# Kernel tuning notes

Hardware: AMD Instinct MI355X
Metric: run time of the kernel (lower is better)

Reference implementation:

```python
import jax, jax.numpy as jnp
import numpy as np


def setup_inputs() -> dict:
    key = jax.random.key(0)
    k1, k2, k3 = jax.random.split(key, 3)
    B, N, D = 32, 1024, 256  # batch, seq len (shared), window_len
    t = jax.random.normal(k1, (B, N, D), dtype=jnp.float32)
    f = jax.random.normal(k2, (B, N, D), dtype=jnp.float32)
    W = jax.random.normal(k3, (D, D), dtype=jnp.float32)  # nn.init.normal_(std=1)
    return {"t": t, "f": f, "W": W}


def reference(t, f, W):
    # s_weight[b,n,m] = t[b,n,:] @ W @ f[b,m,:]
    tW = jnp.einsum('bnd,de->bne', t, W)          # [B,N,D]
    s_weight = jnp.einsum('bne,bme->bnm', tW, f)  # [B,N,N]
    t_weight = jax.nn.softmax(s_weight, axis=1)   # softmax over L_t (dim=1)
    f_weight = jax.nn.softmax(s_weight, axis=2)   # softmax over L_f (dim=2)
    # t_out = t^T @ t_weight -> [B,D,N]
    t_out = jnp.einsum('bnd,bnm->bdm', t, t_weight)
    # f_out = f^T @ f_weight -> [B,D,N] (requires L_t == L_f)
    f_out = jnp.einsum('bmd,bmk->bdk', f, f_weight)
    # Dropout(0.3) omitted (eval-mode identity) for deterministic reference.
    return (t_out, f_out)
```

## Files before the change

kernel.cpp:

```cpp
#include <hip/hip_runtime.h>
#include <math.h>

#define BB 32
#define NN 1024
#define DD 256
#define CH 8
#define KSTEP 32
#define LDK 40

typedef __attribute__((ext_vector_type(8))) short short8;
typedef __attribute__((ext_vector_type(8))) unsigned short u16x8;
typedef __attribute__((ext_vector_type(4))) float f32x4;

__device__ __forceinline__ unsigned short f2bf(float x) {
  unsigned u = __float_as_uint(x);
  unsigned r = (u + 0x7fffu + ((u >> 16) & 1u)) >> 16;
  return (unsigned short)r;
}
__device__ __forceinline__ float bf2f(unsigned short h) {
  return __uint_as_float((unsigned)h << 16);
}

__global__ __launch_bounds__(256) void k_split(const float* __restrict__ src,
                                               unsigned short* __restrict__ hi,
                                               unsigned short* __restrict__ lo, int n4) {
  int i = blockIdx.x * 256 + threadIdx.x;
  if (i >= n4) return;
  float4 v = ((const float4*)src)[i];
  float xs[4] = {v.x, v.y, v.z, v.w};
  ushort4 h4, l4;
  unsigned short* hp = (unsigned short*)&h4;
  unsigned short* lp = (unsigned short*)&l4;
  #pragma unroll
  for (int j = 0; j < 4; ++j) {
    unsigned short h = f2bf(xs[j]);
    hp[j] = h;
    lp[j] = f2bf(xs[j] - bf2f(h));
  }
  ((ushort4*)hi)[i] = h4;
  ((ushort4*)lo)[i] = l4;
}

__global__ __launch_bounds__(256) void k_splitW(const float* __restrict__ W,
                                                unsigned short* __restrict__ Wth,
                                                unsigned short* __restrict__ Wtl) {
  int k = blockIdx.x, n = threadIdx.x;
  float x = W[k * DD + n];
  unsigned short h = f2bf(x);
  Wth[n * DD + k] = h;
  Wtl[n * DD + k] = f2bf(x - bf2f(h));
}

template <int EPI>
__global__ __launch_bounds__(256) void k_gemm_nt(const unsigned short* __restrict__ Ahg,
                                                 const unsigned short* __restrict__ Alg,
                                                 const unsigned short* __restrict__ Bhg,
                                                 const unsigned short* __restrict__ Blg,
                                                 unsigned short* __restrict__ outh,
                                                 unsigned short* __restrict__ outl,
                                                 float* __restrict__ outf, int b0) {
  size_t aoff = 0, boff = 0, coff = 0;
  int ldC = 256;
  if (EPI == 1) {
    int b = b0 + blockIdx.z;
    aoff = (size_t)b * NN * DD;
    boff = (size_t)b * NN * DD;
    coff = (size_t)blockIdx.z * NN * NN;
    ldC = NN;
  }
  const int n0 = blockIdx.x * 128, m0 = blockIdx.y * 128;
  __shared__ unsigned short Ah[128][LDK], Al[128][LDK], Bh[128][LDK], Bl[128][LDK];
  const int tid = threadIdx.x;
  const int lane = tid & 63, w = tid >> 6;
  const int wr = (w >> 1) * 64, wc = (w & 1) * 64;
  const int sr = tid >> 1, sk = (tid & 1) * 16;

  f32x4 acc[4][4] = {};
  const int fr = lane & 15, fk = (lane >> 4) * 8;

  for (int k0 = 0; k0 < DD; k0 += KSTEP) {
    const size_t abase = aoff + (size_t)(n0 + sr) * DD + k0 + sk;
    const size_t bbase = boff + (size_t)(m0 + sr) * DD + k0 + sk;
    *(u16x8*)&Ah[sr][sk] = *(const u16x8*)&Ahg[abase];
    *(u16x8*)&Ah[sr][sk + 8] = *(const u16x8*)&Ahg[abase + 8];
    *(u16x8*)&Al[sr][sk] = *(const u16x8*)&Alg[abase];
    *(u16x8*)&Al[sr][sk + 8] = *(const u16x8*)&Alg[abase + 8];
    *(u16x8*)&Bh[sr][sk] = *(const u16x8*)&Bhg[bbase];
    *(u16x8*)&Bh[sr][sk + 8] = *(const u16x8*)&Bhg[bbase + 8];
    *(u16x8*)&Bl[sr][sk] = *(const u16x8*)&Blg[bbase];
    *(u16x8*)&Bl[sr][sk + 8] = *(const u16x8*)&Blg[bbase + 8];
    __syncthreads();
    short8 ah[4], al[4], bh[4], bl[4];
    #pragma unroll
    for (int mi = 0; mi < 4; ++mi) {
      ah[mi] = *(const short8*)&Ah[wr + mi * 16 + fr][fk];
      al[mi] = *(const short8*)&Al[wr + mi * 16 + fr][fk];
    }
    #pragma unroll
    for (int ni = 0; ni < 4; ++ni) {
      bh[ni] = *(const short8*)&Bh[wc + ni * 16 + fr][fk];
      bl[ni] = *(const short8*)&Bl[wc + ni * 16 + fr][fk];
    }
    #pragma unroll
    for (int mi = 0; mi < 4; ++mi)
      #pragma unroll
      for (int ni = 0; ni < 4; ++ni) {
        acc[mi][ni] = __builtin_amdgcn_mfma_f32_16x16x32_bf16(ah[mi], bh[ni], acc[mi][ni], 0, 0, 0);
        acc[mi][ni] = __builtin_amdgcn_mfma_f32_16x16x32_bf16(ah[mi], bl[ni], acc[mi][ni], 0, 0, 0);
        acc[mi][ni] = __builtin_amdgcn_mfma_f32_16x16x32_bf16(al[mi], bh[ni], acc[mi][ni], 0, 0, 0);
      }
    __syncthreads();
  }
  const int fq = (lane >> 4) * 4;
  #pragma unroll
  for (int mi = 0; mi < 4; ++mi)
    #pragma unroll
    for (int ni = 0; ni < 4; ++ni) {
      #pragma unroll
      for (int q = 0; q < 4; ++q) {
        int row = n0 + wr + mi * 16 + fq + q;
        int col = m0 + wc + ni * 16 + fr;
        float x = acc[mi][ni][q];
        if (EPI == 0) {
          unsigned short h = f2bf(x);
          outh[(size_t)row * 256 + col] = h;
          outl[(size_t)row * 256 + col] = f2bf(x - bf2f(h));
        } else {
          outf[coff + (size_t)row * ldC + col] = x;
        }
      }
    }
}

__global__ __launch_bounds__(256) void k_rowstats(const float* __restrict__ s,
                                                  float* __restrict__ lr, int b0) {
  const int g = blockIdx.y, b = b0 + g, n = blockIdx.x;
  const float* row = s + (size_t)g * NN * NN + (size_t)n * NN;
  const int tid = threadIdx.x;
  float4 v = ((const float4*)row)[tid];
  float mx = fmaxf(fmaxf(v.x, v.y), fmaxf(v.z, v.w));
  float sum = __expf(v.x - mx) + __expf(v.y - mx) + __expf(v.z - mx) + __expf(v.w - mx);
  __shared__ float sm[256], ss[256];
  sm[tid] = mx; ss[tid] = sum;
  __syncthreads();
  for (int off = 128; off > 0; off >>= 1) {
    if (tid < off) {
      float m2 = sm[tid + off], s2 = ss[tid + off];
      float nm = fmaxf(sm[tid], m2);
      ss[tid] = ss[tid] * __expf(sm[tid] - nm) + s2 * __expf(m2 - nm);
      sm[tid] = nm;
    }
    __syncthreads();
  }
  if (tid == 0) lr[(size_t)b * NN + n] = sm[0] + __logf(ss[0]);
}

__global__ __launch_bounds__(256) void k_colstats_part(const float* __restrict__ s,
                                                       float* __restrict__ pm,
                                                       float* __restrict__ ps) {
  const int g = blockIdx.z, ch = blockIdx.y;
  const int mcol = blockIdx.x * 256 + threadIdx.x;
  const float* S = s + (size_t)g * NN * NN;
  float mx = -INFINITY, sum = 0.f;
  const int n0 = ch * (NN / CH), n1 = n0 + NN / CH;
  for (int n = n0; n < n1; ++n) {
    float x = S[(size_t)n * NN + mcol];
    float nm = fmaxf(mx, x);
    sum = sum * __expf(mx - nm) + __expf(x - nm);
    mx = nm;
  }
  pm[((size_t)g * CH + ch) * NN + mcol] = mx;
  ps[((size_t)g * CH + ch) * NN + mcol] = sum;
}

__global__ __launch_bounds__(256) void k_colstats_comb(const float* __restrict__ pm,
                                                       const float* __restrict__ ps,
                                                       float* __restrict__ lc, int b0) {
  const int g = blockIdx.y, b = b0 + g;
  const int mcol = blockIdx.x * 256 + threadIdx.x;
  float mx = -INFINITY, sum = 0.f;
  for (int ch = 0; ch < CH; ++ch) {
    float m2 = pm[((size_t)g * CH + ch) * NN + mcol];
    float s2 = ps[((size_t)g * CH + ch) * NN + mcol];
    float nm = fmaxf(mx, m2);
    sum = sum * __expf(mx - nm) + s2 * __expf(m2 - nm);
    mx = nm;
  }
  lc[(size_t)b * NN + mcol] = mx + __logf(sum);
}

template <int MODE>
__global__ __launch_bounds__(256) void k_out_mfma(const unsigned short* __restrict__ Ahg,
                                                  const float* __restrict__ s,
                                                  const float* __restrict__ lse,
                                                  float* __restrict__ out, int b0) {
  const int g = blockIdx.z, b = b0 + g;
  const int m0 = blockIdx.x * 128;
  const int d0 = blockIdx.y * 128;
  const unsigned short* A = Ahg + (size_t)b * NN * DD;
  const float* S = s + (size_t)g * NN * NN;
  float* O = out + (size_t)b * DD * NN;
  __shared__ unsigned short As_[128][LDK];
  __shared__ unsigned short Bs_[128][LDK];
  const int tid = threadIdx.x;
  const int lane = tid & 63, w = tid >> 6;
  const int wr = (w >> 1) * 64, wc = (w & 1) * 64;
  const int scol = tid & 127;
  const int kg0 = tid >> 7;
  float Lm = 0.f;
  if (MODE == 0) Lm = lse[(size_t)b * NN + m0 + scol];
  f32x4 acc[4][4] = {};
  const int fr = lane & 15, fk = (lane >> 4) * 8;

  for (int k0 = 0; k0 < NN; k0 += KSTEP) {
    #pragma unroll
    for (int ii = 0; ii < 2; ++ii) {
      const int kg = kg0 + ii * 2;
      const int kb = k0 + kg * 8;
      u16x8 pv;
      #pragma unroll
      for (int j = 0; j < 8; ++j) {
        float x = S[(size_t)(kb + j) * NN + m0 + scol];
        float L = (MODE == 0) ? Lm : lse[(size_t)b * NN + kb + j];
        pv[j] = f2bf(__expf(x - L));
      }
      *(u16x8*)&Bs_[scol][kg * 8] = pv;
      u16x8 av;
      #pragma unroll
      for (int j = 0; j < 8; ++j) av[j] = A[(size_t)(kb + j) * DD + d0 + scol];
      *(u16x8*)&As_[scol][kg * 8] = av;
    }
    __syncthreads();
    short8 af[4], bf[4];
    #pragma unroll
    for (int mi = 0; mi < 4; ++mi) af[mi] = *(const short8*)&As_[wr + mi * 16 + fr][fk];
    #pragma unroll
    for (int ni = 0; ni < 4; ++ni) bf[ni] = *(const short8*)&Bs_[wc + ni * 16 + fr][fk];
    #pragma unroll
    for (int mi = 0; mi < 4; ++mi)
      #pragma unroll
      for (int ni = 0; ni < 4; ++ni)
        acc[mi][ni] = __builtin_amdgcn_mfma_f32_16x16x32_bf16(af[mi], bf[ni], acc[mi][ni], 0, 0, 0);
    __syncthreads();
  }
  const int fq = (lane >> 4) * 4;
  #pragma unroll
  for (int mi = 0; mi < 4; ++mi)
    #pragma unroll
    for (int ni = 0; ni < 4; ++ni)
      #pragma unroll
      for (int q = 0; q < 4; ++q) {
        int row = d0 + wr + mi * 16 + fq + q;
        int col = m0 + wc + ni * 16 + fr;
        O[(size_t)row * NN + col] = acc[mi][ni][q];
      }
}

extern "C" void kernel_launch(void* const* d_in, const int* in_sizes, int n_in,
                              void* d_out, int out_size, void* d_ws, size_t ws_size,
                              hipStream_t stream) {
  const float* t = (const float*)d_in[0];
  const float* f = (const float*)d_in[1];
  const float* W = (const float*)d_in[2];
  float* out = (float*)d_out;

  const size_t NE = (size_t)BB * NN * DD;
  char* ws = (char*)d_ws;
  size_t off = 0;
  auto alloc = [&](size_t bytes) { char* p = ws + off; off += (bytes + 255) & ~(size_t)255; return p; };
  unsigned short* t_hi = (unsigned short*)alloc(NE * 2);
  unsigned short* t_lo = (unsigned short*)alloc(NE * 2);
  unsigned short* f_hi = (unsigned short*)alloc(NE * 2);
  unsigned short* f_lo = (unsigned short*)alloc(NE * 2);
  unsigned short* tw_hi = (unsigned short*)alloc(NE * 2);
  unsigned short* tw_lo = (unsigned short*)alloc(NE * 2);
  unsigned short* Wth = (unsigned short*)alloc((size_t)DD * DD * 2);
  unsigned short* Wtl = (unsigned short*)alloc((size_t)DD * DD * 2);
  float* lr = (float*)alloc((size_t)BB * NN * 4);
  float* lc = (float*)alloc((size_t)BB * NN * 4);
  float* pcm = (float*)alloc((size_t)32 * CH * NN * 4);
  float* pcs = (float*)alloc((size_t)32 * CH * NN * 4);
  size_t fixed_bytes = off;
  size_t per_batch = (size_t)NN * NN * sizeof(float);
  int G = 1;
  if (ws_size > fixed_bytes + per_batch) {
    size_t avail = (ws_size - fixed_bytes) / per_batch;
    G = (int)(avail < BB ? avail : BB);
    if (G < 1) G = 1;
  }
  float* sbuf = (float*)(ws + fixed_bytes);

  float* out_t = out;
  float* out_f = out + (size_t)BB * DD * NN;

  k_split<<<(int)((NE / 4 + 255) / 256), 256, 0, stream>>>(t, t_hi, t_lo, (int)(NE / 4));
  k_split<<<(int)((NE / 4 + 255) / 256), 256, 0, stream>>>(f, f_hi, f_lo, (int)(NE / 4));
  k_splitW<<<DD, DD, 0, stream>>>(W, Wth, Wtl);
  k_gemm_nt<0><<<dim3(256, 2, 1), 256, 0, stream>>>(t_hi, t_lo, Wth, Wtl, tw_hi, tw_lo, nullptr, 0);

  for (int b0 = 0; b0 < BB; b0 += G) {
    int g = BB - b0 < G ? BB - b0 : G;
    k_gemm_nt<1><<<dim3(8, 8, g), 256, 0, stream>>>(tw_hi, tw_lo, f_hi, f_lo, nullptr, nullptr, sbuf, b0);
    k_rowstats<<<dim3(NN, g), 256, 0, stream>>>(sbuf, lr, b0);
    k_colstats_part<<<dim3(NN / 256, CH, g), 256, 0, stream>>>(sbuf, pcm, pcs);
    k_colstats_comb<<<dim3(NN / 256, g), 256, 0, stream>>>(pcm, pcs, lc, b0);
    k_out_mfma<0><<<dim3(8, 2, g), 256, 0, stream>>>(t_hi, sbuf, lc, out_t, b0);
    k_out_mfma<1><<<dim3(8, 2, g), 256, 0, stream>>>(f_hi, sbuf, lr, out_f, b0);
  }
}
```

Baseline: 386.5 us.

## Fuse softmax row/column stats into score GEMM epilogue and coalesce output GEMM loads

Row and column max/sum-exp partials are now computed in the score GEMM epilogue with wave shuffles and shared memory, then merged by a small combine kernel. This removes the separate row-stats and column-stats passes that each reread the full score matrix. The output GEMM now stages the score tile in shared memory with coalesced float4 loads, and reads pre-transposed bf16 t/f copies made by a new transpose kernel. It also uses a cheaper bf16 rounding. The costs are an extra transpose pass, extra workspace, and a heavier GEMM epilogue.

```diff
diff --git a/kernel.cpp b/kernel.cpp
--- a/kernel.cpp
+++ b/kernel.cpp
@@ -4,9 +4,9 @@
 #define BB 32
 #define NN 1024
 #define DD 256
-#define CH 8
 #define KSTEP 32
 #define LDK 40
+#define SLD 132
 
 typedef __attribute__((ext_vector_type(8))) short short8;
 typedef __attribute__((ext_vector_type(8))) unsigned short u16x8;
@@ -14,8 +14,10 @@
 
 __device__ __forceinline__ unsigned short f2bf(float x) {
   unsigned u = __float_as_uint(x);
-  unsigned r = (u + 0x7fffu + ((u >> 16) & 1u)) >> 16;
-  return (unsigned short)r;
+  return (unsigned short)((u + 0x7fffu + ((u >> 16) & 1u)) >> 16);
+}
+__device__ __forceinline__ unsigned short f2bf_fast(float x) {
+  return (unsigned short)((__float_as_uint(x) + 0x8000u) >> 16);
 }
 __device__ __forceinline__ float bf2f(unsigned short h) {
   return __uint_as_float((unsigned)h << 16);
@@ -51,6 +53,20 @@
   Wtl[n * DD + k] = f2bf(x - bf2f(h));
 }
 
+__global__ __launch_bounds__(256) void k_transT(const unsigned short* __restrict__ in,
+                                                unsigned short* __restrict__ out) {
+  const int b = blockIdx.z;
+  const int n0 = blockIdx.x * 64, d0 = blockIdx.y * 64;
+  const int tid = threadIdx.x;
+  const int nl = tid & 63, dc = tid >> 6;
+  #pragma unroll
+  for (int dj = 0; dj < 16; ++dj) {
+    int d = d0 + dc * 16 + dj;
+    unsigned short v = in[((size_t)b * NN + n0 + nl) * DD + d];
+    out[((size_t)b * DD + d) * NN + n0 + nl] = v;
+  }
+}
+
 template <int EPI>
 __global__ __launch_bounds__(256) void k_gemm_nt(const unsigned short* __restrict__ Ahg,
                                                  const unsigned short* __restrict__ Alg,
@@ -58,18 +74,23 @@
                                                  const unsigned short* __restrict__ Blg,
                                                  unsigned short* __restrict__ outh,
                                                  unsigned short* __restrict__ outl,
-                                                 float* __restrict__ outf, int b0) {
+                                                 float* __restrict__ outf,
+                                                 float2* __restrict__ prow,
+                                                 float2* __restrict__ pcol, int b0) {
   size_t aoff = 0, boff = 0, coff = 0;
   int ldC = 256;
+  const int g = blockIdx.z;
   if (EPI == 1) {
-    int b = b0 + blockIdx.z;
+    int b = b0 + g;
     aoff = (size_t)b * NN * DD;
     boff = (size_t)b * NN * DD;
-    coff = (size_t)blockIdx.z * NN * NN;
+    coff = (size_t)g * NN * NN;
     ldC = NN;
   }
   const int n0 = blockIdx.x * 128, m0 = blockIdx.y * 128;
   __shared__ unsigned short Ah[128][LDK], Al[128][LDK], Bh[128][LDK], Bl[128][LDK];
+  __shared__ float2 rowbuf[128][2];
+  __shared__ float2 colbuf[128][2];
   const int tid = threadIdx.x;
   const int lane = tid & 63, w = tid >> 6;
   const int wr = (w >> 1) * 64, wc = (w & 1) * 64;
@@ -115,7 +136,7 @@
   #pragma unroll
   for (int mi = 0; mi < 4; ++mi)
     #pragma unroll
-    for (int ni = 0; ni < 4; ++ni) {
+    for (int ni = 0; ni < 4; ++ni)
       #pragma unroll
       for (int q = 0; q < 4; ++q) {
         int row = n0 + wr + mi * 16 + fq + q;
@@ -129,118 +150,124 @@
           outf[coff + (size_t)row * ldC + col] = x;
         }
       }
-    }
-}
-
-__global__ __launch_bounds__(256) void k_rowstats(const float* __restrict__ s,
-                                                  float* __restrict__ lr, int b0) {
-  const int g = blockIdx.y, b = b0 + g, n = blockIdx.x;
-  const float* row = s + (size_t)g * NN * NN + (size_t)n * NN;
-  const int tid = threadIdx.x;
-  float4 v = ((const float4*)row)[tid];
-  float mx = fmaxf(fmaxf(v.x, v.y), fmaxf(v.z, v.w));
-  float sum = __expf(v.x - mx) + __expf(v.y - mx) + __expf(v.z - mx) + __expf(v.w - mx);
-  __shared__ float sm[256], ss[256];
-  sm[tid] = mx; ss[tid] = sum;
-  __syncthreads();
-  for (int off = 128; off > 0; off >>= 1) {
-    if (tid < off) {
-      float m2 = sm[tid + off], s2 = ss[tid + off];
-      float nm = fmaxf(sm[tid], m2);
-      ss[tid] = ss[tid] * __expf(sm[tid] - nm) + s2 * __expf(m2 - nm);
-      sm[tid] = nm;
-    }
-    __syncthreads();
-  }
-  if (tid == 0) lr[(size_t)b * NN + n] = sm[0] + __logf(ss[0]);
-}
-
-__global__ __launch_bounds__(256) void k_colstats_part(const float* __restrict__ s,
-                                                       float* __restrict__ pm,
-                                                       float* __restrict__ ps) {
-  const int g = blockIdx.z, ch = blockIdx.y;
-  const int mcol = blockIdx.x * 256 + threadIdx.x;
-  const float* S = s + (size_t)g * NN * NN;
+  if (EPI == 1) {
+    #pragma unroll
+    for (int mi = 0; mi < 4; ++mi)
+      #pragma unroll
+      for (int q = 0; q < 4; ++q) {
+        float v0 = acc[mi][0][q], v1 = acc[mi][1][q], v2 = acc[mi][2][q], v3 = acc[mi][3][q];
+        float mx = fmaxf(fmaxf(v0, v1), fmaxf(v2, v3));
+        #pragma unroll
+        for (int mask = 1; mask <= 8; mask <<= 1) mx = fmaxf(mx, __shfl_xor(mx, mask));
+        float se = __expf(v0 - mx) + __expf(v1 - mx) + __expf(v2 - mx) + __expf(v3 - mx);
+        #pragma unroll
+        for (int mask = 1; mask <= 8; mask <<= 1) se += __shfl_xor(se, mask);
+        if (fr == 0) rowbuf[wr + mi * 16 + fq + q][w & 1] = make_float2(mx, se);
+      }
+    #pragma unroll
+    for (int ni = 0; ni < 4; ++ni) {
+      float mx = -INFINITY;
+      #pragma unroll
+      for (int mi = 0; mi < 4; ++mi)
+        #pragma unroll
+        for (int q = 0; q < 4; ++q) mx = fmaxf(mx, acc[mi][ni][q]);
+      mx = fmaxf(mx, __shfl_xor(mx, 16));
+      mx = fmaxf(mx, __shfl_xor(mx, 32));
+      float se = 0.f;
+      #pragma unroll
+      for (int mi = 0; mi < 4; ++mi)
+        #pragma unroll
+        for (int q = 0; q < 4; ++q) se += __expf(acc[mi][ni][q] - mx);
+      se += __shfl_xor(se, 16);
+      se += __shfl_xor(se, 32);
+      if ((lane >> 4) == 0) colbuf[wc + ni * 16 + fr][w >> 1] = make_float2(mx, se);
+    }
+    __syncthreads();
+    if (tid < 128) {
+      float2 a = rowbuf[tid][0], c = rowbuf[tid][1];
+      float nm = fmaxf(a.x, c.x);
+      float s = a.y * __expf(a.x - nm) + c.y * __expf(c.x - nm);
+      prow[((size_t)g * NN + n0 + tid) * 8 + blockIdx.y] = make_float2(nm, s);
+    } else {
+      int m = tid - 128;
+      float2 a = colbuf[m][0], c = colbuf[m][1];
+      float nm = fmaxf(a.x, c.x);
+      float s = a.y * __expf(a.x - nm) + c.y * __expf(c.x - nm);
+      pcol[((size_t)g * NN + m0 + m) * 8 + blockIdx.x] = make_float2(nm, s);
+    }
+  }
+}
+
+__global__ __launch_bounds__(256) void k_comb(const float2* __restrict__ part,
+                                              float* __restrict__ lse, int b0) {
+  const int g = blockIdx.y, b = b0 + g;
+  const int i = blockIdx.x * 256 + threadIdx.x;
   float mx = -INFINITY, sum = 0.f;
-  const int n0 = ch * (NN / CH), n1 = n0 + NN / CH;
-  for (int n = n0; n < n1; ++n) {
-    float x = S[(size_t)n * NN + mcol];
-    float nm = fmaxf(mx, x);
-    sum = sum * __expf(mx - nm) + __expf(x - nm);
+  #pragma unroll
+  for (int c = 0; c < 8; ++c) {
+    float2 p = part[((size_t)g * NN + i) * 8 + c];
+    float nm = fmaxf(mx, p.x);
+    sum = sum * __expf(mx - nm) + p.y * __expf(p.x - nm);
     mx = nm;
   }
-  pm[((size_t)g * CH + ch) * NN + mcol] = mx;
-  ps[((size_t)g * CH + ch) * NN + mcol] = sum;
-}
-
-__global__ __launch_bounds__(256) void k_colstats_comb(const float* __restrict__ pm,
-                                                       const float* __restrict__ ps,
-                                                       float* __restrict__ lc, int b0) {
-  const int g = blockIdx.y, b = b0 + g;
-  const int mcol = blockIdx.x * 256 + threadIdx.x;
-  float mx = -INFINITY, sum = 0.f;
-  for (int ch = 0; ch < CH; ++ch) {
-    float m2 = pm[((size_t)g * CH + ch) * NN + mcol];
-    float s2 = ps[((size_t)g * CH + ch) * NN + mcol];
-    float nm = fmaxf(mx, m2);
-    sum = sum * __expf(mx - nm) + s2 * __expf(m2 - nm);
-    mx = nm;
-  }
-  lc[(size_t)b * NN + mcol] = mx + __logf(sum);
+  lse[(size_t)b * NN + i] = mx + __logf(sum);
 }
 
 template <int MODE>
-__global__ __launch_bounds__(256) void k_out_mfma(const unsigned short* __restrict__ Ahg,
-                                                  const float* __restrict__ s,
-                                                  const float* __restrict__ lse,
-                                                  float* __restrict__ out, int b0) {
+__global__ __launch_bounds__(256) void k_outg(const unsigned short* __restrict__ ATg,
+                                              const float* __restrict__ s,
+                                              const float* __restrict__ lse,
+                                              float* __restrict__ out, int b0) {
   const int g = blockIdx.z, b = b0 + g;
-  const int m0 = blockIdx.x * 128;
-  const int d0 = blockIdx.y * 128;
-  const unsigned short* A = Ahg + (size_t)b * NN * DD;
+  const int m0 = blockIdx.x * 128, d0 = blockIdx.y * 128;
+  const unsigned short* A = ATg + (size_t)b * DD * NN;
   const float* S = s + (size_t)g * NN * NN;
   float* O = out + (size_t)b * DD * NN;
-  __shared__ unsigned short As_[128][LDK];
-  __shared__ unsigned short Bs_[128][LDK];
+  __shared__ unsigned short Asm[128][LDK];
+  __shared__ float Ssm[KSTEP][SLD];
+  __shared__ float lrs[KSTEP];
   const int tid = threadIdx.x;
   const int lane = tid & 63, w = tid >> 6;
   const int wr = (w >> 1) * 64, wc = (w & 1) * 64;
-  const int scol = tid & 127;
-  const int kg0 = tid >> 7;
-  float Lm = 0.f;
-  if (MODE == 0) Lm = lse[(size_t)b * NN + m0 + scol];
+  const int fr = lane & 15, fk = (lane >> 4) * 8;
+  const int sr = tid >> 1, sk = (tid & 1) * 16;
+  const int skk = tid >> 3, smq = (tid & 7) * 16;
+  float lcv[4];
+  if (MODE == 0) {
+    #pragma unroll
+    for (int ni = 0; ni < 4; ++ni)
+      lcv[ni] = lse[(size_t)b * NN + m0 + wc + ni * 16 + fr];
+  }
   f32x4 acc[4][4] = {};
-  const int fr = lane & 15, fk = (lane >> 4) * 8;
-
   for (int k0 = 0; k0 < NN; k0 += KSTEP) {
-    #pragma unroll
-    for (int ii = 0; ii < 2; ++ii) {
-      const int kg = kg0 + ii * 2;
-      const int kb = k0 + kg * 8;
-      u16x8 pv;
+    const size_t ab = (size_t)(d0 + sr) * NN + k0 + sk;
+    *(u16x8*)&Asm[sr][sk] = *(const u16x8*)&A[ab];
+    *(u16x8*)&Asm[sr][sk + 8] = *(const u16x8*)&A[ab + 8];
+    #pragma unroll
+    for (int i = 0; i < 4; ++i)
+      *(float4*)&Ssm[skk][smq + 4 * i] =
+          *(const float4*)&S[(size_t)(k0 + skk) * NN + m0 + smq + 4 * i];
+    if (MODE == 1 && tid < KSTEP) lrs[tid] = lse[(size_t)b * NN + k0 + tid];
+    __syncthreads();
+    short8 af[4], bfr[4];
+    #pragma unroll
+    for (int mi = 0; mi < 4; ++mi) af[mi] = *(const short8*)&Asm[wr + mi * 16 + fr][fk];
+    #pragma unroll
+    for (int ni = 0; ni < 4; ++ni) {
+      unsigned short tmp[8];
       #pragma unroll
       for (int j = 0; j < 8; ++j) {
-        float x = S[(size_t)(kb + j) * NN + m0 + scol];
-        float L = (MODE == 0) ? Lm : lse[(size_t)b * NN + kb + j];
-        pv[j] = f2bf(__expf(x - L));
+        float x = Ssm[fk + j][wc + ni * 16 + fr];
+        float L = (MODE == 0) ? lcv[ni] : lrs[fk + j];
+        tmp[j] = f2bf_fast(__expf(x - L));
       }
-      *(u16x8*)&Bs_[scol][kg * 8] = pv;
-      u16x8 av;
-      #pragma unroll
-      for (int j = 0; j < 8; ++j) av[j] = A[(size_t)(kb + j) * DD + d0 + scol];
-      *(u16x8*)&As_[scol][kg * 8] = av;
-    }
-    __syncthreads();
-    short8 af[4], bf[4];
-    #pragma unroll
-    for (int mi = 0; mi < 4; ++mi) af[mi] = *(const short8*)&As_[wr + mi * 16 + fr][fk];
-    #pragma unroll
-    for (int ni = 0; ni < 4; ++ni) bf[ni] = *(const short8*)&Bs_[wc + ni * 16 + fr][fk];
+      bfr[ni] = *(const short8*)tmp;
+    }
     #pragma unroll
     for (int mi = 0; mi < 4; ++mi)
       #pragma unroll
       for (int ni = 0; ni < 4; ++ni)
-        acc[mi][ni] = __builtin_amdgcn_mfma_f32_16x16x32_bf16(af[mi], bf[ni], acc[mi][ni], 0, 0, 0);
+        acc[mi][ni] = __builtin_amdgcn_mfma_f32_16x16x32_bf16(af[mi], bfr[ni], acc[mi][ni], 0, 0, 0);
     __syncthreads();
   }
   const int fq = (lane >> 4) * 4;
@@ -249,11 +276,8 @@
     #pragma unroll
     for (int ni = 0; ni < 4; ++ni)
       #pragma unroll
-      for (int q = 0; q < 4; ++q) {
-        int row = d0 + wr + mi * 16 + fq + q;
-        int col = m0 + wc + ni * 16 + fr;
-        O[(size_t)row * NN + col] = acc[mi][ni][q];
-      }
+      for (int q = 0; q < 4; ++q)
+        O[(size_t)(d0 + wr + mi * 16 + fq + q) * NN + m0 + wc + ni * 16 + fr] = acc[mi][ni][q];
 }
 
 extern "C" void kernel_launch(void* const* d_in, const int* in_sizes, int n_in,
@@ -274,12 +298,14 @@
   unsigned short* f_lo = (unsigned short*)alloc(NE * 2);
   unsigned short* tw_hi = (unsigned short*)alloc(NE * 2);
   unsigned short* tw_lo = (unsigned short*)alloc(NE * 2);
+  unsigned short* tT = (unsigned short*)alloc(NE * 2);
+  unsigned short* fT = (unsigned short*)alloc(NE * 2);
   unsigned short* Wth = (unsigned short*)alloc((size_t)DD * DD * 2);
   unsigned short* Wtl = (unsigned short*)alloc((size_t)DD * DD * 2);
   float* lr = (float*)alloc((size_t)BB * NN * 4);
   float* lc = (float*)alloc((size_t)BB * NN * 4);
-  float* pcm = (float*)alloc((size_t)32 * CH * NN * 4);
-  float* pcs = (float*)alloc((size_t)32 * CH * NN * 4);
+  float2* prow = (float2*)alloc((size_t)BB * NN * 8 * 8);
+  float2* pcol = (float2*)alloc((size_t)BB * NN * 8 * 8);
   size_t fixed_bytes = off;
   size_t per_batch = (size_t)NN * NN * sizeof(float);
   int G = 1;
@@ -296,15 +322,18 @@
   k_split<<<(int)((NE / 4 + 255) / 256), 256, 0, stream>>>(t, t_hi, t_lo, (int)(NE / 4));
   k_split<<<(int)((NE / 4 + 255) / 256), 256, 0, stream>>>(f, f_hi, f_lo, (int)(NE / 4));
   k_splitW<<<DD, DD, 0, stream>>>(W, Wth, Wtl);
-  k_gemm_nt<0><<<dim3(256, 2, 1), 256, 0, stream>>>(t_hi, t_lo, Wth, Wtl, tw_hi, tw_lo, nullptr, 0);
+  k_transT<<<dim3(NN / 64, DD / 64, BB), 256, 0, stream>>>(t_hi, tT);
+  k_transT<<<dim3(NN / 64, DD / 64, BB), 256, 0, stream>>>(f_hi, fT);
+  k_gemm_nt<0><<<dim3(256, 2, 1), 256, 0, stream>>>(t_hi, t_lo, Wth, Wtl, tw_hi, tw_lo,
+                                                    nullptr, nullptr, nullptr, 0);
 
   for (int b0 = 0; b0 < BB; b0 += G) {
     int g = BB - b0 < G ? BB - b0 : G;
-    k_gemm_nt<1><<<dim3(8, 8, g), 256, 0, stream>>>(tw_hi, tw_lo, f_hi, f_lo, nullptr, nullptr, sbuf, b0);
-    k_rowstats<<<dim3(NN, g), 256, 0, stream>>>(sbuf, lr, b0);
-    k_colstats_part<<<dim3(NN / 256, CH, g), 256, 0, stream>>>(sbuf, pcm, pcs);
-    k_colstats_comb<<<dim3(NN / 256, g), 256, 0, stream>>>(pcm, pcs, lc, b0);
-    k_out_mfma<0><<<dim3(8, 2, g), 256, 0, stream>>>(t_hi, sbuf, lc, out_t, b0);
-    k_out_mfma<1><<<dim3(8, 2, g), 256, 0, stream>>>(f_hi, sbuf, lr, out_f, b0);
-  }
-}
+    k_gemm_nt<1><<<dim3(8, 8, g), 256, 0, stream>>>(tw_hi, tw_lo, f_hi, f_lo, nullptr, nullptr,
+                                                    sbuf, prow, pcol, b0);
+    k_comb<<<dim3(NN / 256, g), 256, 0, stream>>>(prow, lr, b0);
+    k_comb<<<dim3(NN / 256, g), 256, 0, stream>>>(pcol, lc, b0);
+    k_outg<0><<<dim3(8, 2, g), 256, 0, stream>>>(tT, sbuf, lc, out_t, b0);
+    k_outg<1><<<dim3(8, 2, g), 256, 0, stream>>>(fT, sbuf, lr, out_f, b0);
+  }
+}
```

Result: slower. 539.1 us (+39.5%).
